# Kernel optimization log

Measured on AMD Instinct MI355X. Metric: run time of the kernel, lower is better.

Reference implementation:

```python
import jax, jax.numpy as jnp
import numpy as np

B_SZ, L_SEQ, H_CH, N_ST = 8, 4096, 256, 64


def setup_inputs() -> dict:
    key = jax.random.key(0)
    ks = jax.random.split(key, 12)
    rn = lambda k, s, sc=1.0: jax.random.normal(k, s, jnp.float32) * sc
    inp = {
        'x': rn(ks[0], (B_SZ, L_SEQ, H_CH)),
        # stable DPLR spectrum: Re(Lambda) < 0, HiPPO-like imaginary ladder
        'Lambda_re': -(jnp.abs(rn(ks[1], (N_ST,))) + 0.1),
        'Lambda_im': jnp.pi * jnp.arange(N_ST, dtype=jnp.float32),
        'P_re': rn(ks[2], (N_ST,), N_ST ** -0.5),
        'P_im': rn(ks[3], (N_ST,), N_ST ** -0.5),
        'Q_re': rn(ks[4], (N_ST,), N_ST ** -0.5),
        'Q_im': rn(ks[5], (N_ST,), N_ST ** -0.5),
        'B_re': rn(ks[6], (N_ST,), N_ST ** -0.5),
        'B_im': rn(ks[7], (N_ST,), N_ST ** -0.5),
        'C_re': rn(ks[8], (H_CH, N_ST), N_ST ** -0.5),
        'C_im': rn(ks[9], (H_CH, N_ST), N_ST ** -0.5),
        'step': jnp.ones((1,), jnp.float32) * 1e-3,
        'D': jnp.zeros((1,), jnp.float32),
        'W_fc': rn(ks[10], (H_CH, H_CH), H_CH ** -0.5),
        'b_fc': jnp.zeros((H_CH,), jnp.float32),
        'ln_g': jnp.ones((H_CH,), jnp.float32),
        'ln_b': jnp.zeros((H_CH,), jnp.float32),
    }
    return inp


def _dplr_kernel(Lambda_re, Lambda_im, P_re, P_im, Q_re, Q_im, B_re, B_im, C_re, C_im, step, L):
    # S4 DPLR generating function evaluated at the L roots of unity (torch_get_K_derta).
    Lam = (Lambda_re + 1j * Lambda_im).astype(jnp.complex64)  # (N,)
    Pc = (P_re + 1j * P_im).astype(jnp.complex64)
    Qc = (Q_re + 1j * Q_im).astype(jnp.complex64)
    Bc = (B_re + 1j * B_im).astype(jnp.complex64)
    Cc = (C_re + 1j * C_im).astype(jnp.complex64)  # (H, N)
    k = jnp.arange(L, dtype=jnp.float32)
    Omega = jnp.exp((-2j * jnp.pi) * (k / L)).astype(jnp.complex64)  # (L,)
    c = 2.0 / (1.0 + Omega)
    g = (2.0 / step[0]) * (1.0 - Omega) / (1.0 + Omega)  # bilinear transform points, (L,)
    inv = 1.0 / (g[:, None] - Lam[None, :])  # Cauchy matrix, (L, N)
    k00 = jnp.einsum('hn,ln->hl', Cc * Bc[None, :], inv)  # (H, L)
    k01 = jnp.einsum('hn,ln->hl', Cc * Pc[None, :], inv)
    k10 = jnp.einsum('n,ln->l', Qc * Bc, inv)  # (L,)
    k11 = jnp.einsum('n,ln->l', Qc * Pc, inv)
    atRoots = c[None, :] * (k00 - k01 * (k10 / (1.0 + k11))[None, :])  # Woodbury correction
    K = jnp.fft.ifft(atRoots, axis=-1).real  # (H, L)
    return K.astype(jnp.float32)


def reference(x, Lambda_re, Lambda_im, P_re, P_im, Q_re, Q_im, B_re, B_im, C_re, C_im, step, D, W_fc, b_fc, ln_g, ln_b):
    Bsz, L, H = x.shape
    step = jnp.maximum(step, 1e-6)
    K = _dplr_kernel(Lambda_re, Lambda_im, P_re, P_im, Q_re, Q_im, B_re, B_im, C_re, C_im, step, L)  # (H, L)
    # causal FFT convolution per channel (torch_convolution with fft=True)
    n = 2 * L
    Kf = jnp.fft.rfft(K, n=n, axis=-1)           # (H, F)
    uf = jnp.fft.rfft(x, n=n, axis=1)            # (B, F, H)
    h1 = jnp.fft.irfft(uf * Kf.T[None], n=n, axis=1)[:, :L, :]
    y1 = jax.nn.gelu(h1 + D * x, approximate=False)  # mult_activation='gelu'
    y2 = jax.nn.gelu(y1 @ W_fc.T + b_fc, approximate=False)  # fc + final_act
    y2 = y2 + x  # skip
    mu = jnp.mean(y2, axis=-1, keepdims=True)
    var = jnp.var(y2, axis=-1, keepdims=True)
    y = (y2 - mu) / jnp.sqrt(var + 1e-5) * ln_g + ln_b  # LayerNorm; dropout p=0
    h_ratio = jnp.max(jnp.abs(y), axis=1) / (jnp.max(jnp.abs(x), axis=1) + 1e-6)  # (B, H)
    return y, h_ratio
```

## Files before the change

### kernel.cpp

```cpp
#include <hip/hip_runtime.h>
#include <math.h>

typedef float2 cf;
typedef float vf2 __attribute__((ext_vector_type(2)));
typedef __attribute__((ext_vector_type(8))) short bf16x8;
typedef __attribute__((ext_vector_type(4))) float f32x4;

__device__ __forceinline__ cf cmk(float x, float y){ cf r; r.x=x; r.y=y; return r; }

__device__ __forceinline__ cf cad(cf a, cf b){
  vf2 av, bv, rv;
  av.x = a.x; av.y = a.y; bv.x = b.x; bv.y = b.y;
  asm("v_pk_add_f32 %0, %1, %2" : "=v"(rv) : "v"(av), "v"(bv));
  return cmk(rv.x, rv.y);
}
__device__ __forceinline__ cf csb(cf a, cf b){
  vf2 av, bv, rv;
  av.x = a.x; av.y = a.y; bv.x = b.x; bv.y = b.y;
  asm("v_pk_add_f32 %0, %1, %2 neg_lo:[0,1] neg_hi:[0,1]" : "=v"(rv) : "v"(av), "v"(bv));
  return cmk(rv.x, rv.y);
}
__device__ __forceinline__ cf cml(cf a, cf b){
  vf2 av, bv, rv;
  av.x = a.x; av.y = a.y; bv.x = b.x; bv.y = b.y;
  asm("v_pk_mul_f32 %0, %1, %2 op_sel:[0,0] op_sel_hi:[0,1]\n\t"
      "v_pk_fma_f32 %0, %1, %2, %0 op_sel:[1,1,0] op_sel_hi:[1,0,1] neg_lo:[1,0,0]"
      : "=&v"(rv) : "v"(av), "v"(bv));
  return cmk(rv.x, rv.y);
}

__device__ __forceinline__ cf cjg(cf a){ return cmk(a.x, -a.y); }
__device__ __forceinline__ cf crcp(cf d){ float r = 1.0f/(d.x*d.x + d.y*d.y); return cmk(d.x*r, -d.y*r); }
__device__ __forceinline__ cf cdv(cf n, cf d){ return cml(n, crcp(d)); }
__device__ __forceinline__ float geluf(float z){ return 0.5f*z*(1.0f + erff(z*0.70710678118654752f)); }

__device__ __forceinline__ cf twid(float f, float sign){
  float h = f * 0.5f;
  float s = __builtin_amdgcn_sinf(h);
  float c0 = __builtin_amdgcn_cosf(h);
  return cmk(c0, sign * s);
}

__device__ __forceinline__ void bfsplit(float v, ushort* h, ushort* l){
  unsigned u = __float_as_uint(v);
  unsigned hr = (u + 0x7FFFu + ((u >> 16) & 1u)) & 0xFFFF0000u;
  *h = (ushort)(hr >> 16);
  float lv = v - __uint_as_float(hr);
  unsigned u2 = __float_as_uint(lv);
  *l = (ushort)((u2 + 0x7FFFu + ((u2 >> 16) & 1u)) >> 16);
}

__device__ __forceinline__ void dif4q(cf& q0, cf& q1, cf& q2, cf& q3, cf w1, float sign){
  cf w2 = cml(w1, w1);
  cf a1 = cad(q0, q2);
  cf c1 = cml(csb(q0, q2), w1);
  cf b1 = cad(q1, q3);
  cf d1 = cml(csb(q1, q3), cmk(-sign*w1.y, sign*w1.x));
  q0 = cad(a1, b1);
  q1 = cml(csb(a1, b1), w2);
  q2 = cad(c1, d1);
  q3 = cml(csb(c1, d1), w2);
}
__device__ __forceinline__ void dit4q(cf& q0, cf& q1, cf& q2, cf& q3, cf w1, float sign){
  cf w2 = cml(w1, w1);
  cf t1 = cml(q1, w2);
  cf a1 = cad(q0, t1), b1 = csb(q0, t1);
  cf t2 = cml(q3, w2);
  cf c1 = cad(q2, t2), d1 = csb(q2, t2);
  cf v1 = cml(c1, w1);
  cf v2 = cml(d1, cmk(-sign*w1.y, sign*w1.x));
  q0 = cad(a1, v1);
  q2 = csb(a1, v1);
  q1 = cad(b1, v2);
  q3 = csb(b1, v2);
}
__device__ __forceinline__ void dif4q0(cf& q0, cf& q1, cf& q2, cf& q3, float sign){
  cf a1 = cad(q0, q2), c1 = csb(q0, q2);
  cf b1 = cad(q1, q3), d0 = csb(q1, q3);
  cf d1 = cmk(-sign*d0.y, sign*d0.x);
  q0 = cad(a1, b1); q1 = csb(a1, b1);
  q2 = cad(c1, d1); q3 = csb(c1, d1);
}
__device__ __forceinline__ void dit4q0(cf& q0, cf& q1, cf& q2, cf& q3, float sign){
  cf a1 = cad(q0, q1), b1 = csb(q0, q1);
  cf c1 = cad(q2, q3), d0 = csb(q2, q3);
  cf v2 = cmk(-sign*d0.y, sign*d0.x);
  q0 = cad(a1, c1); q2 = csb(a1, c1);
  q1 = cad(b1, v2); q3 = csb(b1, v2);
}

__device__ __forceinline__ int brev12(int x){ return (int)(__brev((unsigned)x) >> 20); }
__device__ __forceinline__ int brev13(int x){ return (int)(__brev((unsigned)x) >> 19); }
__device__ __forceinline__ int pidx(int n){ return n + 2*(n>>5); }

template<int N, int SSTART, int TP>
__device__ void fft_dif_r4(cf* __restrict__ a, float sign){
  #pragma unroll
  for (int s = SSTART; s >= 1; s >>= 2){
    __syncthreads();
    #pragma unroll
    for (int g = 0; g < (N >> 2) / TP; g++){
      int w = (int)threadIdx.x + g * TP;
      int j = w & (s - 1);
      int base = ((w & ~(s - 1)) << 2) | j;
      cf A0 = a[base], B0 = a[base + s], C0 = a[base + 2*s], D0 = a[base + 3*s];
      cf w1 = twid((float)j / (float)(2 * s), sign);
      cf w2 = cml(w1, w1);
      cf a1 = cad(A0, C0);
      cf c1 = cml(csb(A0, C0), w1);
      cf b1 = cad(B0, D0);
      cf d1 = cml(csb(B0, D0), cmk(-sign * w1.y, sign * w1.x));
      a[base]         = cad(a1, b1);
      a[base + s]     = cml(csb(a1, b1), w2);
      a[base + 2*s]   = cad(c1, d1);
      a[base + 3*s]   = cml(csb(c1, d1), w2);
    }
  }
  if constexpr ((__builtin_ctz(N) & 1) == 1){
    __syncthreads();
    #pragma unroll
    for (int g = 0; g < (N >> 1) / TP; g++){
      int w = (int)threadIdx.x + g * TP;
      int i = w << 1;
      cf u = a[i], v = a[i + 1];
      a[i] = cad(u, v);
      a[i + 1] = csb(u, v);
    }
  }
  __syncthreads();
}

template<int N, int TP>
__device__ void fft_dit_r4(cf* __restrict__ a, float sign){
  if constexpr ((__builtin_ctz(N) & 1) == 1){
    __syncthreads();
    #pragma unroll
    for (int g = 0; g < (N >> 1) / TP; g++){
      int w = (int)threadIdx.x + g * TP;
      int i = w << 1;
      cf u = a[i], v = a[i + 1];
      a[i] = cad(u, v);
      a[i + 1] = csb(u, v);
    }
  }
  constexpr int S0 = ((__builtin_ctz(N) & 1) == 1) ? 2 : 1;
  #pragma unroll
  for (int s = S0; s <= (N >> 2); s <<= 2){
    __syncthreads();
    #pragma unroll
    for (int g = 0; g < (N >> 2) / TP; g++){
      int w = (int)threadIdx.x + g * TP;
      int j = w & (s - 1);
      int base = ((w & ~(s - 1)) << 2) | j;
      cf A0 = a[base], B0 = a[base + s], C0 = a[base + 2*s], D0 = a[base + 3*s];
      cf w1 = twid((float)j / (float)(2 * s), sign);
      cf w2 = cml(w1, w1);
      cf t1 = cml(B0, w2);
      cf a1 = cad(A0, t1), b1 = csb(A0, t1);
      cf t2 = cml(D0, w2);
      cf c1 = cad(C0, t2), d1 = csb(C0, t2);
      cf v1 = cml(c1, w1);
      cf v2 = cml(d1, cmk(-sign * w1.y, sign * w1.x));
      a[base]         = cad(a1, v1);
      a[base + 2*s]   = csb(a1, v1);
      a[base + s]     = cad(b1, v2);
      a[base + 3*s]   = csb(b1, v2);
    }
  }
  __syncthreads();
}

template<int TP>
__device__ void dif8192_pad_stage(cf* __restrict__ a, float sign){
  __syncthreads();
  #pragma unroll
  for (int g = 0; g < 2048 / TP; g++){
    int w = (int)threadIdx.x + g * TP;
    cf A0 = a[w], B0 = a[w + 2048];
    cf w1 = twid((float)w * (1.0f / 4096.0f), sign);
    cf w2 = cml(w1, w1);
    cf c1 = cml(A0, w1);
    cf d1 = cml(B0, cmk(-sign * w1.y, sign * w1.x));
    a[w]        = cad(A0, B0);
    a[w + 2048] = cml(csb(A0, B0), w2);
    a[w + 4096] = cad(c1, d1);
    a[w + 6144] = cml(csb(c1, d1), w2);
  }
}

__global__ __launch_bounds__(256) void k_transpose_x(const float* __restrict__ x,
                                                     float* __restrict__ xT,
                                                     unsigned* __restrict__ xmax){
  __shared__ float tile[64][65];
  __shared__ float red[64][4];
  int b = blockIdx.z;
  int t0 = blockIdx.x * 64;
  int h0 = blockIdx.y * 64;
  int hc = threadIdx.x & 63, tg = threadIdx.x >> 6;
  float pmax = 0.0f;
  #pragma unroll
  for (int q = 0; q < 16; q++){
    int tr = tg + q * 4;
    float v = x[((size_t)(b * 4096 + t0 + tr)) * 256 + h0 + hc];
    tile[tr][hc] = v;
    pmax = fmaxf(pmax, fabsf(v));
  }
  red[hc][tg] = pmax;
  __syncthreads();
  if (threadIdx.x < 64){
    float m = fmaxf(fmaxf(red[threadIdx.x][0], red[threadIdx.x][1]),
                    fmaxf(red[threadIdx.x][2], red[threadIdx.x][3]));
    atomicMax(&xmax[b * 256 + h0 + threadIdx.x], __float_as_uint(m));
  }
  #pragma unroll
  for (int q = 0; q < 16; q++){
    int hr = tg + q * 4;
    xT[((size_t)(b * 256 + h0 + hr)) * 4096 + t0 + hc] = tile[hc][hr];
  }
}

__global__ void k_wsplit(const float* __restrict__ W, ushort* __restrict__ Wh, ushort* __restrict__ Wl,
                         unsigned* __restrict__ xmax, unsigned* __restrict__ ymax,
                         const float* __restrict__ Cr, const float* __restrict__ Ci,
                         const float* __restrict__ Br, const float* __restrict__ Bi,
                         const float* __restrict__ Pr, const float* __restrict__ Pi,
                         cf* __restrict__ CBt, cf* __restrict__ CPt){
  int i = blockIdx.x * 256 + threadIdx.x;
  if (i < 2048){ xmax[i] = 0u; ymax[i] = 0u; }
  if (i < 16384){
    int n = i >> 8, h = i & 255;
    cf cc = cmk(Cr[h * 64 + n], Ci[h * 64 + n]);
    CBt[i] = cml(cc, cmk(Br[n], Bi[n]));
    CPt[i] = cml(cc, cmk(Pr[n], Pi[n]));
  }
  ushort h, l;
  bfsplit(W[i], &h, &l);
  Wh[i] = h; Wl[i] = l;
}

__global__ __launch_bounds__(256, 2) void k_cauchy(
    const float* __restrict__ Lr, const float* __restrict__ Li,
    const float* __restrict__ Pr, const float* __restrict__ Pi,
    const float* __restrict__ Qr, const float* __restrict__ Qi,
    const float* __restrict__ Br, const float* __restrict__ Bi,
    const cf* __restrict__ CBt, const cf* __restrict__ CPt,
    const float* __restrict__ stepp, cf* __restrict__ A)
{
  __shared__ cf sLam[64], sQB[64], sQP[64];
  __shared__ cf sInv[64][8];
  __shared__ cf sWood[8], sC[8], sG[8];
  int tid = threadIdx.x;
  int l0 = blockIdx.x * 8;
  float stepv = fmaxf(stepp[0], 1e-6f);
  if (tid < 64){
    cf lam = cmk(Lr[tid], Li[tid]);
    cf b = cmk(Br[tid], Bi[tid]);
    cf p = cmk(Pr[tid], Pi[tid]);
    cf q = cmk(Qr[tid], Qi[tid]);
    sLam[tid] = lam;
    sQB[tid] = cml(q, b);
    sQP[tid] = cml(q, p);
  }
  __syncthreads();
  if (tid < 8){
    int l = l0 + tid;
    float ang = -6.2831855f * ((float)l * (1.0f / 4096.0f));
    cf Om = cmk(cosf(ang), sinf(ang));
    cf den = cmk(1.0f + Om.x, Om.y);
    cf num = cmk(1.0f - Om.x, -Om.y);
    cf rden = crcp(den);
    sC[tid] = cml(cmk(2.0f, 0.0f), rden);
    cf g = cml(num, rden);
    float sc = 2.0f / stepv;
    sG[tid] = cmk(g.x * sc, g.y * sc);
  }
  __syncthreads();
  for (int it = tid; it < 512; it += 256){
    int n = it >> 3, ll = it & 7;
    sInv[n][ll] = crcp(csb(sG[ll], sLam[n]));
  }
  __syncthreads();
  if (tid < 8){
    cf k10 = cmk(0,0), k11 = cmk(0,0);
    for (int n = 0; n < 64; n++){
      k10 = cad(k10, cml(sQB[n], sInv[n][tid]));
      k11 = cad(k11, cml(sQP[n], sInv[n][tid]));
    }
    sWood[tid] = cdv(k10, cmk(1.0f + k11.x, k11.y));
  }
  __syncthreads();
  int h = tid;
  cf a0[8], a1[8];
  #pragma unroll
  for (int ll = 0; ll < 8; ll++){ a0[ll] = cmk(0,0); a1[ll] = cmk(0,0); }
  for (int n = 0; n < 64; n++){
    cf cb = CBt[n * 256 + h];
    cf cp = CPt[n * 256 + h];
    #pragma unroll
    for (int ll = 0; ll < 8; ll++){
      cf iv = sInv[n][ll];
      a0[ll] = cad(a0[ll], cml(cb, iv));
      a1[ll] = cad(a1[ll], cml(cp, iv));
    }
  }
  cf* dst = A + (size_t)h * 4096 + l0;
  #pragma unroll
  for (int ll = 0; ll < 8; ll++){
    dst[ll] = cml(sC[ll], csb(a0[ll], cml(a1[ll], sWood[ll])));
  }
}

__global__ __launch_bounds__(1024) void k_kf(const cf* __restrict__ A, float4* __restrict__ Sab){
  extern __shared__ cf c[];
  int hp = blockIdx.x, tid = threadIdx.x;
  const cf* a1p = A + (size_t)(2 * hp) * 4096;
  const cf* a2p = a1p + 4096;
  for (int l = tid; l < 4096; l += 1024){
    int r = brev12(l);
    cf u = a1p[l], w = a2p[l];
    c[r] = cmk(u.x - w.y, u.y + w.x);
  }
  fft_dit_r4<4096, 1024>(c, 1.0f);
  float k1[4], k2[4];
  #pragma unroll
  for (int q = 0; q < 4; q++){
    cf w = c[tid + q * 1024];
    k1[q] = w.x * (1.0f / 4096.0f);
    k2[q] = w.y * (1.0f / 4096.0f);
  }
  __syncthreads();
  #pragma unroll
  for (int q = 0; q < 4; q++) c[tid + q * 1024] = cmk(k1[q], k2[q]);
  dif8192_pad_stage<1024>(c, -1.0f);
  fft_dif_r4<8192, 512, 1024>(c, -1.0f);
  float4* rec = Sab + (size_t)hp * 4097;
  const float sc = 0.5f * 0.5f * (1.0f / 8192.0f);
  #pragma unroll
  for (int q8 = 0; q8 < 4; q8++){
    int t = tid + 1024 * q8;
    int p = t << 1;
    int k = brev13(p);
    int qq = brev13((8192 - k) & 8191);
    cf Zp = c[p], Zq = c[qq];
    float K1x = (Zp.x + Zq.x), K1y = (Zp.y - Zq.y);
    float dx  = (Zp.x - Zq.x), dy  = (Zp.y + Zq.y);
    float K2x = dy, K2y = -dx;
    rec[t] = make_float4((K1x + K2x) * sc, (K1y + K2y) * sc,
                         (K1x - K2x) * sc, (K1y - K2y) * sc);
  }
  if (tid == 0){
    cf Z1 = c[1];
    float K1x = 2.0f * Z1.x, K2x = 2.0f * Z1.y;
    rec[4096] = make_float4((K1x + K2x) * sc, 0.0f, (K1x - K2x) * sc, 0.0f);
  }
}

__global__ __launch_bounds__(256) void k_conv(const float* __restrict__ xT,
                                              const float4* __restrict__ Sab,
                                              const float* __restrict__ Dp,
                                              ushort* __restrict__ y1h,
                                              ushort* __restrict__ y1l){
  __shared__ __align__(16) cf c[8704];
  int blk = blockIdx.x;
  int b = blk >> 7, hp = blk & 127;
  int t = threadIdx.x;
  int lo4 = t & 15, hiT = t >> 4;
  int base0 = lo4 + ((hiT << 1) << 8);
  int base1 = lo4 + ((((hiT << 1) | 1)) << 8);
  int cb0 = pidx((t << 1) << 4);
  int cb1 = pidx(((t << 1) | 1) << 4);
  const float* xs1 = xT + ((size_t)(b * 256 + 2 * hp)) * 4096;
  const float* xs2 = xs1 + 4096;
  cf v[32];
  #pragma unroll
  for (int r = 0; r < 16; r++){
    int n = t + 256 * r;
    v[r] = cmk(xs1[n], xs2[n]);
  }
  #pragma unroll
  for (int r = 0; r < 16; r++)
    v[r + 16] = cml(v[r], twid((float)(t + 256 * r) * (1.0f / 4096.0f), -1.0f));
  #pragma unroll
  for (int r0 = 0; r0 < 4; r0++){
    cf w1 = twid((float)(t + 256 * r0) * (1.0f / 2048.0f), -1.0f);
    dif4q(v[r0], v[r0 + 4], v[r0 + 8], v[r0 + 12], w1, -1.0f);
    dif4q(v[16 + r0], v[16 + r0 + 4], v[16 + r0 + 8], v[16 + r0 + 12], w1, -1.0f);
  }
  {
    cf w1 = twid((float)t * (1.0f / 512.0f), -1.0f);
    #pragma unroll
    for (int g = 0; g < 32; g += 4)
      dif4q(v[g], v[g + 1], v[g + 2], v[g + 3], w1, -1.0f);
  }
  #pragma unroll
  for (int r = 0; r < 32; r++) c[pidx(t + 256 * r)] = v[r];
  __syncthreads();
  #pragma unroll
  for (int u = 0; u < 16; u++){
    v[u]      = c[pidx(base0 + (u << 4))];
    v[16 + u] = c[pidx(base1 + (u << 4))];
  }
  #pragma unroll
  for (int u0 = 0; u0 < 4; u0++){
    cf w1 = twid((float)(lo4 + (u0 << 4)) * (1.0f / 128.0f), -1.0f);
    dif4q(v[u0], v[u0 + 4], v[u0 + 8], v[u0 + 12], w1, -1.0f);
    dif4q(v[16 + u0], v[16 + u0 + 4], v[16 + u0 + 8], v[16 + u0 + 12], w1, -1.0f);
  }
  {
    cf w1 = twid((float)lo4 * (1.0f / 32.0f), -1.0f);
    #pragma unroll
    for (int g = 0; g < 32; g += 4)
      dif4q(v[g], v[g + 1], v[g + 2], v[g + 3], w1, -1.0f);
  }
  #pragma unroll
  for (int u = 0; u < 16; u++){
    c[pidx(base0 + (u << 4))] = v[u];
    c[pidx(base1 + (u << 4))] = v[16 + u];
  }
  __syncthreads();
  #pragma unroll
  for (int k = 0; k < 8; k++){
    float4 q0 = *(const float4*)&c[cb0 + 2 * k];
    float4 q1 = *(const float4*)&c[cb1 + 2 * k];
    v[2 * k]      = cmk(q0.x, q0.y); v[2 * k + 1]      = cmk(q0.z, q0.w);
    v[16 + 2 * k] = cmk(q1.x, q1.y); v[16 + 2 * k + 1] = cmk(q1.z, q1.w);
  }
  #pragma unroll
  for (int u0 = 0; u0 < 4; u0++){
    cf w1 = twid((float)u0 * 0.125f, -1.0f);
    dif4q(v[u0], v[u0 + 4], v[u0 + 8], v[u0 + 12], w1, -1.0f);
    dif4q(v[16 + u0], v[16 + u0 + 4], v[16 + u0 + 8], v[16 + u0 + 12], w1, -1.0f);
  }
  #pragma unroll
  for (int g = 0; g < 32; g += 4) dif4q0(v[g], v[g + 1], v[g + 2], v[g + 3], -1.0f);
  #pragma unroll
  for (int k = 0; k < 8; k++){
    *(float4*)&c[cb0 + 2 * k] = make_float4(v[2*k].x, v[2*k].y, v[2*k+1].x, v[2*k+1].y);
    *(float4*)&c[cb1 + 2 * k] = make_float4(v[16+2*k].x, v[16+2*k].y, v[16+2*k+1].x, v[16+2*k+1].y);
  }
  __syncthreads();
  {
    const float4* rec = Sab + (size_t)hp * 4097;
    #pragma unroll
    for (int q8 = 0; q8 < 16; q8++){
      int th = t + 256 * q8;
      int p = th << 1;
      int k = brev13(p);
      int qq = brev13((8192 - k) & 8191);
      int pi = pidx(p), qi = pidx(qq);
      cf Zp = c[pi], Zq = c[qi];
      float4 r0 = rec[th];
      cf Sap = cmk(r0.x, r0.y), Sbp = cmk(r0.z, r0.w);
      c[pi] = cad(cml(Zp, Sap), cml(cjg(Zq), Sbp));
      c[qi] = cad(cml(Zq, cjg(Sap)), cml(cjg(Zp), cjg(Sbp)));
    }
    if (t == 0){
      float4 e = rec[4096];
      cf Z1 = c[pidx(1)];
      c[pidx(1)] = cad(cml(Z1, cmk(e.x, e.y)), cml(cjg(Z1), cmk(e.z, e.w)));
    }
  }
  __syncthreads();
  #pragma unroll
  for (int k = 0; k < 8; k++){
    float4 q0 = *(const float4*)&c[cb0 + 2 * k];
    float4 q1 = *(const float4*)&c[cb1 + 2 * k];
    v[2 * k]      = cmk(q0.x, q0.y); v[2 * k + 1]      = cmk(q0.z, q0.w);
    v[16 + 2 * k] = cmk(q1.x, q1.y); v[16 + 2 * k + 1] = cmk(q1.z, q1.w);
  }
  #pragma unroll
  for (int g = 0; g < 32; g += 4) dit4q0(v[g], v[g + 1], v[g + 2], v[g + 3], 1.0f);
  #pragma unroll
  for (int u0 = 0; u0 < 4; u0++){
    cf w1 = twid((float)u0 * 0.125f, 1.0f);
    dit4q(v[u0], v[u0 + 4], v[u0 + 8], v[u0 + 12], w1, 1.0f);
    dit4q(v[16 + u0], v[16 + u0 + 4], v[16 + u0 + 8], v[16 + u0 + 12], w1, 1.0f);
  }
  #pragma unroll
  for (int k = 0; k < 8; k++){
    *(float4*)&c[cb0 + 2 * k] = make_float4(v[2*k].x, v[2*k].y, v[2*k+1].x, v[2*k+1].y);
    *(float4*)&c[cb1 + 2 * k] = make_float4(v[16+2*k].x, v[16+2*k].y, v[16+2*k+1].x, v[16+2*k+1].y);
  }
  __syncthreads();
  #pragma unroll
  for (int u = 0; u < 16; u++){
    v[u]      = c[pidx(base0 + (u << 4))];
    v[16 + u] = c[pidx(base1 + (u << 4))];
  }
  {
    cf w1 = twid((float)lo4 * (1.0f / 32.0f), 1.0f);
    #pragma unroll
    for (int g = 0; g < 32; g += 4)
      dit4q(v[g], v[g + 1], v[g + 2], v[g + 3], w1, 1.0f);
  }
  #pragma unroll
  for (int u0 = 0; u0 < 4; u0++){
    cf w1 = twid((float)(lo4 + (u0 << 4)) * (1.0f / 128.0f), 1.0f);
    dit4q(v[u0], v[u0 + 4], v[u0 + 8], v[u0 + 12], w1, 1.0f);
    dit4q(v[16 + u0], v[16 + u0 + 4], v[16 + u0 + 8], v[16 + u0 + 12], w1, 1.0f);
  }
  #pragma unroll
  for (int u = 0; u < 16; u++){
    c[pidx(base0 + (u << 4))] = v[u];
    c[pidx(base1 + (u << 4))] = v[16 + u];
  }
  __syncthreads();
  #pragma unroll
  for (int r = 0; r < 32; r++) v[r] = c[pidx(t + 256 * r)];
  {
    cf w1 = twid((float)t * (1.0f / 512.0f), 1.0f);
    #pragma unroll
    for (int g = 0; g < 32; g += 4)
      dit4q(v[g], v[g + 1], v[g + 2], v[g + 3], w1, 1.0f);
  }
  #pragma unroll
  for (int r0 = 0; r0 < 4; r0++){
    cf w1 = twid((float)(t + 256 * r0) * (1.0f / 2048.0f), 1.0f);
    dit4q(v[r0], v[r0 + 4], v[r0 + 8], v[r0 + 12], w1, 1.0f);
    dit4q(v[16 + r0], v[16 + r0 + 4], v[16 + r0 + 8], v[16 + r0 + 12], w1, 1.0f);
  }
  float Dv = Dp[0];
  size_t base = ((size_t)(b * 256 + 2 * hp)) * 4096;
  #pragma unroll
  for (int r = 0; r < 16; r++){
    int n = t + 256 * r;
    cf w = cad(v[r], cml(v[r + 16], twid((float)n * (1.0f / 4096.0f), 1.0f)));
    float z1 = geluf(fmaf(Dv, xs1[n], w.x));
    float z2 = geluf(fmaf(Dv, xs2[n], w.y));
    ushort h0, l0, h1u, l1;
    bfsplit(z1, &h0, &l0);
    bfsplit(z2, &h1u, &l1);
    y1h[base + n] = h0;         y1l[base + n] = l0;
    y1h[base + 4096 + n] = h1u; y1l[base + 4096 + n] = l1;
  }
}

__global__ __launch_bounds__(256, 3) void k_gemm_ln(
    const ushort* __restrict__ y1h, const ushort* __restrict__ y1l,
    const ushort* __restrict__ Wh, const ushort* __restrict__ Wl,
    const float* __restrict__ bfc, const float* __restrict__ x,
    const float* __restrict__ lng, const float* __restrict__ lnb,
    float* __restrict__ yout, unsigned* __restrict__ ymax)
{
  __shared__ ushort sY[2][64 * 40];
  __shared__ float red1[64][4], red2[64][4];
  int tid = threadIdx.x;
  int l = tid & 63;
  int w = tid >> 6;
  int blk = blockIdx.x;
  int b = blk >> 6;
  int t0 = (blk & 63) * 64;
  int g = l >> 4, cc = l & 15;

  f32x4 acc[4][4];
  #pragma unroll
  for (int m = 0; m < 4; m++)
    #pragma unroll
    for (int n = 0; n < 4; n++)
      acc[m][n] = (f32x4){0.0f, 0.0f, 0.0f, 0.0f};

  int kk = tid >> 3, ts = (tid & 7) * 8;

  #pragma unroll 1
  for (int kc = 0; kc < 256; kc += 32){
    __syncthreads();
    {
      size_t gb = ((size_t)(b * 256 + kc + kk)) * 4096 + t0 + ts;
      float4 vh = *(const float4*)(y1h + gb);
      float4 vl = *(const float4*)(y1l + gb);
      const ushort* ph = (const ushort*)&vh;
      const ushort* pl = (const ushort*)&vl;
      int kblk = kk >> 3, kin = kk & 7;
      #pragma unroll
      for (int e = 0; e < 8; e++){
        int t = ts + e;
        int idx = t * 40 + ((kblk ^ ((t >> 3) & 3)) << 3) + kin;
        sY[0][idx] = ph[e];
        sY[1][idx] = pl[e];
      }
    }
    __syncthreads();
    bf16x8 afh[4], afl[4];
    #pragma unroll
    for (int m = 0; m < 4; m++){
      int t = m * 16 + cc;
      int idx = t * 40 + ((g ^ ((t >> 3) & 3)) << 3);
      afh[m] = *(bf16x8*)&sY[0][idx];
      afl[m] = *(bf16x8*)&sY[1][idx];
    }
    #pragma unroll
    for (int n = 0; n < 4; n++){
      size_t wj = (size_t)(w * 64 + n * 16 + cc) * 256 + kc + g * 8;
      bf16x8 bh = *(const bf16x8*)(Wh + wj);
      bf16x8 bl = *(const bf16x8*)(Wl + wj);
      #pragma unroll
      for (int m = 0; m < 4; m++){
        acc[m][n] = __builtin_amdgcn_mfma_f32_16x16x32_bf16(afh[m], bh, acc[m][n], 0, 0, 0);
        acc[m][n] = __builtin_amdgcn_mfma_f32_16x16x32_bf16(afh[m], bl, acc[m][n], 0, 0, 0);
        acc[m][n] = __builtin_amdgcn_mfma_f32_16x16x32_bf16(afl[m], bh, acc[m][n], 0, 0, 0);
      }
    }
  }

  float bj[4], gj[4], lj[4];
  #pragma unroll
  for (int n = 0; n < 4; n++){
    int j = w * 64 + n * 16 + cc;
    bj[n] = bfc[j]; gj[n] = lng[j]; lj[n] = lnb[j];
  }
  #pragma unroll
  for (int m = 0; m < 4; m++){
    #pragma unroll
    for (int r = 0; r < 4; r++){
      int tl = m * 16 + g * 4 + r;
      size_t rowb = ((size_t)(b * 4096 + t0 + tl)) * 256;
      float ss = 0.0f, sq = 0.0f;
      #pragma unroll
      for (int n = 0; n < 4; n++){
        float z = geluf(acc[m][n][r] + bj[n]) + x[rowb + w * 64 + n * 16 + cc];
        acc[m][n][r] = z;
        ss += z; sq = fmaf(z, z, sq);
      }
      #pragma unroll
      for (int msk = 1; msk < 16; msk <<= 1){
        ss += __shfl_xor(ss, msk);
        sq += __shfl_xor(sq, msk);
      }
      if (cc == 0){ red1[tl][w] = ss; red2[tl][w] = sq; }
    }
  }
  __syncthreads();
  float jm[4] = {0.0f, 0.0f, 0.0f, 0.0f};
  #pragma unroll
  for (int m = 0; m < 4; m++){
    #pragma unroll
    for (int r = 0; r < 4; r++){
      int tl = m * 16 + g * 4 + r;
      float ts1 = red1[tl][0] + red1[tl][1] + red1[tl][2] + red1[tl][3];
      float ts2 = red2[tl][0] + red2[tl][1] + red2[tl][2] + red2[tl][3];
      float mu = ts1 * (1.0f / 256.0f);
      float var = ts2 * (1.0f / 256.0f) - mu * mu;
      float rstd = rsqrtf(var + 1e-5f);
      size_t rowb = ((size_t)(b * 4096 + t0 + tl)) * 256;
      #pragma unroll
      for (int n = 0; n < 4; n++){
        float yv = (acc[m][n][r] - mu) * rstd * gj[n] + lj[n];
        yout[rowb + w * 64 + n * 16 + cc] = yv;
        jm[n] = fmaxf(jm[n], fabsf(yv));
      }
    }
  }
  #pragma unroll
  for (int n = 0; n < 4; n++){
    jm[n] = fmaxf(jm[n], __shfl_xor(jm[n], 16));
    jm[n] = fmaxf(jm[n], __shfl_xor(jm[n], 32));
  }
  if (g == 0){
    #pragma unroll
    for (int n = 0; n < 4; n++)
      atomicMax(&ymax[b * 256 + w * 64 + n * 16 + cc], __float_as_uint(jm[n]));
  }
}

__global__ void k_ratio(const unsigned* __restrict__ ymax, const unsigned* __restrict__ xmax,
                        float* __restrict__ out){
  int i = blockIdx.x * 256 + threadIdx.x;
  if (i < 2048){
    float ym = __uint_as_float(ymax[i]);
    float xm = __uint_as_float(xmax[i]);
    out[8388608 + i] = ym / (xm + 1e-6f);
  }
}

extern "C" void kernel_launch(void* const* d_in, const int* in_sizes, int n_in,
                              void* d_out, int out_size, void* d_ws, size_t ws_size,
                              hipStream_t stream)
{
  const float* x    = (const float*)d_in[0];
  const float* Lr   = (const float*)d_in[1];
  const float* Li   = (const float*)d_in[2];
  const float* Pr   = (const float*)d_in[3];
  const float* Pi   = (const float*)d_in[4];
  const float* Qr   = (const float*)d_in[5];
  const float* Qi   = (const float*)d_in[6];
  const float* Br   = (const float*)d_in[7];
  const float* Bi   = (const float*)d_in[8];
  const float* Cr   = (const float*)d_in[9];
  const float* Ci   = (const float*)d_in[10];
  const float* stp  = (const float*)d_in[11];
  const float* Dp   = (const float*)d_in[12];
  const float* Wfc  = (const float*)d_in[13];
  const float* bfc  = (const float*)d_in[14];
  const float* lng  = (const float*)d_in[15];
  const float* lnb  = (const float*)d_in[16];

  char* ws = (char*)d_ws;
  float*    xT   = (float*)(ws);
  float4*   Sab  = (float4*)(ws + ((size_t)32 << 20));
  cf*       A    = (cf*)(ws + ((size_t)41 << 20));
  ushort*   y1h  = (ushort*)(ws + ((size_t)41 << 20));
  ushort*   y1l  = (ushort*)(ws + ((size_t)57 << 20));
  ushort*   Wh   = (ushort*)(ws + ((size_t)73 << 20));
  ushort*   Wl   = (ushort*)(ws + ((size_t)73 << 20) + (128u << 10));
  unsigned* xmax = (unsigned*)(ws + ((size_t)73 << 20) + (256u << 10));
  unsigned* ymax = xmax + 2048;
  cf*       CBt  = (cf*)(ws + ((size_t)74 << 20));
  cf*       CPt  = (cf*)(ws + ((size_t)74 << 20) + (128u << 10));

  k_wsplit<<<256, 256, 0, stream>>>(Wfc, Wh, Wl, xmax, ymax, Cr, Ci, Br, Bi, Pr, Pi, CBt, CPt);
  dim3 gt(64, 4, 8);
  k_transpose_x<<<gt, 256, 0, stream>>>(x, xT, xmax);
  k_cauchy<<<512, 256, 0, stream>>>(Lr, Li, Pr, Pi, Qr, Qi, Br, Bi, CBt, CPt, stp, A);
  k_kf<<<128, 1024, 65536, stream>>>(A, Sab);
  k_conv<<<1024, 256, 0, stream>>>(xT, Sab, Dp, y1h, y1l);
  k_gemm_ln<<<512, 256, 0, stream>>>(y1h, y1l, Wh, Wl, bfc, x, lng, lnb, (float*)d_out, ymax);
  k_ratio<<<8, 256, 0, stream>>>(ymax, xmax, (float*)d_out);
}
```

Baseline: 173.2 us.

## Restructure FFT convolution kernel to 512 threads with shuffle-based radix-2 stage

```diff
diff --git a/kernel.cpp b/kernel.cpp
--- a/kernel.cpp
+++ b/kernel.cpp
@@ -39,6 +39,10 @@
   float s = __builtin_amdgcn_sinf(h);
   float c0 = __builtin_amdgcn_cosf(h);
   return cmk(c0, sign * s);
+}
+
+__device__ __forceinline__ cf shflx(cf v, int m){
+  return cmk(__shfl_xor(v.x, m), __shfl_xor(v.y, m));
 }
 
 __device__ __forceinline__ void bfsplit(float v, ushort* h, ushort* l){
@@ -91,7 +95,7 @@
 
 __device__ __forceinline__ int brev12(int x){ return (int)(__brev((unsigned)x) >> 20); }
 __device__ __forceinline__ int brev13(int x){ return (int)(__brev((unsigned)x) >> 19); }
-__device__ __forceinline__ int pidx(int n){ return n + 2*(n>>5); }
+__device__ __forceinline__ int pidx(int n){ return n + 6*(n>>5); }
 
 template<int N, int SSTART, int TP>
 __device__ void fft_dif_r4(cf* __restrict__ a, float sign){
@@ -355,95 +359,94 @@
   }
 }
 
-__global__ __launch_bounds__(256) void k_conv(const float* __restrict__ xT,
+__global__ __launch_bounds__(512) void k_conv(const float* __restrict__ xT,
                                               const float4* __restrict__ Sab,
                                               const float* __restrict__ Dp,
                                               ushort* __restrict__ y1h,
                                               ushort* __restrict__ y1l){
-  __shared__ __align__(16) cf c[8704];
+  __shared__ __align__(16) cf c[9728];
   int blk = blockIdx.x;
   int b = blk >> 7, hp = blk & 127;
   int t = threadIdx.x;
-  int lo4 = t & 15, hiT = t >> 4;
-  int base0 = lo4 + ((hiT << 1) << 8);
-  int base1 = lo4 + ((((hiT << 1) | 1)) << 8);
-  int cb0 = pidx((t << 1) << 4);
-  int cb1 = pidx(((t << 1) | 1) << 4);
+  int cl = t & 31;
+  int m1b = (t >> 5) * 512 + cl;
+  int cb  = pidx(t << 4);
   const float* xs1 = xT + ((size_t)(b * 256 + 2 * hp)) * 4096;
   const float* xs2 = xs1 + 4096;
-  cf v[32];
-  #pragma unroll
-  for (int r = 0; r < 16; r++){
-    int n = t + 256 * r;
+  cf v[16];
+  #pragma unroll
+  for (int r = 0; r < 8; r++){
+    int n = t + 512 * r;
     v[r] = cmk(xs1[n], xs2[n]);
   }
   #pragma unroll
-  for (int r = 0; r < 16; r++)
-    v[r + 16] = cml(v[r], twid((float)(t + 256 * r) * (1.0f / 4096.0f), -1.0f));
-  #pragma unroll
-  for (int r0 = 0; r0 < 4; r0++){
-    cf w1 = twid((float)(t + 256 * r0) * (1.0f / 2048.0f), -1.0f);
-    dif4q(v[r0], v[r0 + 4], v[r0 + 8], v[r0 + 12], w1, -1.0f);
-    dif4q(v[16 + r0], v[16 + r0 + 4], v[16 + r0 + 8], v[16 + r0 + 12], w1, -1.0f);
+  for (int r = 0; r < 8; r++)
+    v[r + 8] = cml(v[r], twid((float)(t + 512 * r) * (1.0f / 4096.0f), -1.0f));
+  #pragma unroll
+  for (int r0 = 0; r0 < 2; r0++){
+    cf w1 = twid((float)(t + 512 * r0) * (1.0f / 2048.0f), -1.0f);
+    dif4q(v[r0], v[r0 + 2], v[r0 + 4], v[r0 + 6], w1, -1.0f);
+    dif4q(v[8 + r0], v[8 + r0 + 2], v[8 + r0 + 4], v[8 + r0 + 6], w1, -1.0f);
   }
   {
-    cf w1 = twid((float)t * (1.0f / 512.0f), -1.0f);
-    #pragma unroll
-    for (int g = 0; g < 32; g += 4)
+    cf tw = twid((float)t * (1.0f / 512.0f), -1.0f);
+    #pragma unroll
+    for (int g = 0; g < 16; g += 2){
+      cf lo = cad(v[g], v[g + 1]);
+      cf hi = cml(csb(v[g], v[g + 1]), tw);
+      v[g] = lo; v[g + 1] = hi;
+    }
+  }
+  #pragma unroll
+  for (int r = 0; r < 16; r++) c[pidx(t + 512 * r)] = v[r];
+  __syncthreads();
+  #pragma unroll
+  for (int u = 0; u < 16; u++) v[u] = c[pidx(m1b + u * 32)];
+  #pragma unroll
+  for (int u0 = 0; u0 < 4; u0++){
+    cf w1 = twid((float)(cl + 32 * u0) * (1.0f / 256.0f), -1.0f);
+    dif4q(v[u0], v[u0 + 4], v[u0 + 8], v[u0 + 12], w1, -1.0f);
+  }
+  {
+    cf w1 = twid((float)cl * (1.0f / 64.0f), -1.0f);
+    #pragma unroll
+    for (int g = 0; g < 16; g += 4)
       dif4q(v[g], v[g + 1], v[g + 2], v[g + 3], w1, -1.0f);
   }
   #pragma unroll
-  for (int r = 0; r < 32; r++) c[pidx(t + 256 * r)] = v[r];
-  __syncthreads();
-  #pragma unroll
-  for (int u = 0; u < 16; u++){
-    v[u]      = c[pidx(base0 + (u << 4))];
-    v[16 + u] = c[pidx(base1 + (u << 4))];
-  }
-  #pragma unroll
-  for (int u0 = 0; u0 < 4; u0++){
-    cf w1 = twid((float)(lo4 + (u0 << 4)) * (1.0f / 128.0f), -1.0f);
-    dif4q(v[u0], v[u0 + 4], v[u0 + 8], v[u0 + 12], w1, -1.0f);
-    dif4q(v[16 + u0], v[16 + u0 + 4], v[16 + u0 + 8], v[16 + u0 + 12], w1, -1.0f);
+  for (int u = 0; u < 16; u++) c[pidx(m1b + u * 32)] = v[u];
+  __syncthreads();
+  #pragma unroll
+  for (int k = 0; k < 8; k++){
+    float4 q0 = *(const float4*)&c[cb + 2 * k];
+    v[2 * k]     = cmk(q0.x, q0.y);
+    v[2 * k + 1] = cmk(q0.z, q0.w);
   }
   {
-    cf w1 = twid((float)lo4 * (1.0f / 32.0f), -1.0f);
-    #pragma unroll
-    for (int g = 0; g < 32; g += 4)
-      dif4q(v[g], v[g + 1], v[g + 2], v[g + 3], w1, -1.0f);
-  }
-  #pragma unroll
-  for (int u = 0; u < 16; u++){
-    c[pidx(base0 + (u << 4))] = v[u];
-    c[pidx(base1 + (u << 4))] = v[16 + u];
-  }
-  __syncthreads();
-  #pragma unroll
-  for (int k = 0; k < 8; k++){
-    float4 q0 = *(const float4*)&c[cb0 + 2 * k];
-    float4 q1 = *(const float4*)&c[cb1 + 2 * k];
-    v[2 * k]      = cmk(q0.x, q0.y); v[2 * k + 1]      = cmk(q0.z, q0.w);
-    v[16 + 2 * k] = cmk(q1.x, q1.y); v[16 + 2 * k + 1] = cmk(q1.z, q1.w);
+    bool hb = (t & 1) != 0;
+    #pragma unroll
+    for (int u2 = 0; u2 < 16; u2++){
+      cf o = shflx(v[u2], 1);
+      cf tw = twid((float)u2 * (1.0f / 16.0f), -1.0f);
+      v[u2] = hb ? cml(csb(o, v[u2]), tw) : cad(v[u2], o);
+    }
   }
   #pragma unroll
   for (int u0 = 0; u0 < 4; u0++){
     cf w1 = twid((float)u0 * 0.125f, -1.0f);
     dif4q(v[u0], v[u0 + 4], v[u0 + 8], v[u0 + 12], w1, -1.0f);
-    dif4q(v[16 + u0], v[16 + u0 + 4], v[16 + u0 + 8], v[16 + u0 + 12], w1, -1.0f);
-  }
-  #pragma unroll
-  for (int g = 0; g < 32; g += 4) dif4q0(v[g], v[g + 1], v[g + 2], v[g + 3], -1.0f);
-  #pragma unroll
-  for (int k = 0; k < 8; k++){
-    *(float4*)&c[cb0 + 2 * k] = make_float4(v[2*k].x, v[2*k].y, v[2*k+1].x, v[2*k+1].y);
-    *(float4*)&c[cb1 + 2 * k] = make_float4(v[16+2*k].x, v[16+2*k].y, v[16+2*k+1].x, v[16+2*k+1].y);
-  }
+  }
+  #pragma unroll
+  for (int g = 0; g < 16; g += 4) dif4q0(v[g], v[g + 1], v[g + 2], v[g + 3], -1.0f);
+  #pragma unroll
+  for (int k = 0; k < 8; k++)
+    *(float4*)&c[cb + 2 * k] = make_float4(v[2*k].x, v[2*k].y, v[2*k+1].x, v[2*k+1].y);
   __syncthreads();
   {
     const float4* rec = Sab + (size_t)hp * 4097;
     #pragma unroll
-    for (int q8 = 0; q8 < 16; q8++){
-      int th = t + 256 * q8;
+    for (int q8 = 0; q8 < 8; q8++){
+      int th = t + 512 * q8;
       int p = th << 1;
       int k = brev13(p);
       int qq = brev13((8192 - k) & 8191);
@@ -463,68 +466,71 @@
   __syncthreads();
   #pragma unroll
   for (int k = 0; k < 8; k++){
-    float4 q0 = *(const float4*)&c[cb0 + 2 * k];
-    float4 q1 = *(const float4*)&c[cb1 + 2 * k];
-    v[2 * k]      = cmk(q0.x, q0.y); v[2 * k + 1]      = cmk(q0.z, q0.w);
-    v[16 + 2 * k] = cmk(q1.x, q1.y); v[16 + 2 * k + 1] = cmk(q1.z, q1.w);
-  }
-  #pragma unroll
-  for (int g = 0; g < 32; g += 4) dit4q0(v[g], v[g + 1], v[g + 2], v[g + 3], 1.0f);
+    float4 q0 = *(const float4*)&c[cb + 2 * k];
+    v[2 * k]     = cmk(q0.x, q0.y);
+    v[2 * k + 1] = cmk(q0.z, q0.w);
+  }
+  #pragma unroll
+  for (int g = 0; g < 16; g += 4) dit4q0(v[g], v[g + 1], v[g + 2], v[g + 3], 1.0f);
   #pragma unroll
   for (int u0 = 0; u0 < 4; u0++){
     cf w1 = twid((float)u0 * 0.125f, 1.0f);
     dit4q(v[u0], v[u0 + 4], v[u0 + 8], v[u0 + 12], w1, 1.0f);
-    dit4q(v[16 + u0], v[16 + u0 + 4], v[16 + u0 + 8], v[16 + u0 + 12], w1, 1.0f);
-  }
-  #pragma unroll
-  for (int k = 0; k < 8; k++){
-    *(float4*)&c[cb0 + 2 * k] = make_float4(v[2*k].x, v[2*k].y, v[2*k+1].x, v[2*k+1].y);
-    *(float4*)&c[cb1 + 2 * k] = make_float4(v[16+2*k].x, v[16+2*k].y, v[16+2*k+1].x, v[16+2*k+1].y);
-  }
-  __syncthreads();
-  #pragma unroll
-  for (int u = 0; u < 16; u++){
-    v[u]      = c[pidx(base0 + (u << 4))];
-    v[16 + u] = c[pidx(base1 + (u << 4))];
   }
   {
-    cf w1 = twid((float)lo4 * (1.0f / 32.0f), 1.0f);
-    #pragma unroll
-    for (int g = 0; g < 32; g += 4)
+    bool hb = (t & 1) != 0;
+    #pragma unroll
+    for (int u2 = 0; u2 < 16; u2++){
+      cf o = shflx(v[u2], 1);
+      cf w = twid((float)u2 * (1.0f / 16.0f), 1.0f);
+      cf whv = cml(w, hb ? v[u2] : o);
+      v[u2] = hb ? csb(o, whv) : cad(v[u2], whv);
+    }
+  }
+  #pragma unroll
+  for (int k = 0; k < 8; k++)
+    *(float4*)&c[cb + 2 * k] = make_float4(v[2*k].x, v[2*k].y, v[2*k+1].x, v[2*k+1].y);
+  __syncthreads();
+  #pragma unroll
+  for (int u = 0; u < 16; u++) v[u] = c[pidx(m1b + u * 32)];
+  {
+    cf w1 = twid((float)cl * (1.0f / 64.0f), 1.0f);
+    #pragma unroll
+    for (int g = 0; g < 16; g += 4)
       dit4q(v[g], v[g + 1], v[g + 2], v[g + 3], w1, 1.0f);
   }
   #pragma unroll
   for (int u0 = 0; u0 < 4; u0++){
-    cf w1 = twid((float)(lo4 + (u0 << 4)) * (1.0f / 128.0f), 1.0f);
+    cf w1 = twid((float)(cl + 32 * u0) * (1.0f / 256.0f), 1.0f);
     dit4q(v[u0], v[u0 + 4], v[u0 + 8], v[u0 + 12], w1, 1.0f);
-    dit4q(v[16 + u0], v[16 + u0 + 4], v[16 + u0 + 8], v[16 + u0 + 12], w1, 1.0f);
-  }
-  #pragma unroll
-  for (int u = 0; u < 16; u++){
-    c[pidx(base0 + (u << 4))] = v[u];
-    c[pidx(base1 + (u << 4))] = v[16 + u];
-  }
-  __syncthreads();
-  #pragma unroll
-  for (int r = 0; r < 32; r++) v[r] = c[pidx(t + 256 * r)];
+  }
+  #pragma unroll
+  for (int u = 0; u < 16; u++) c[pidx(m1b + u * 32)] = v[u];
+  __syncthreads();
+  #pragma unroll
+  for (int r = 0; r < 16; r++) v[r] = c[pidx(t + 512 * r)];
   {
-    cf w1 = twid((float)t * (1.0f / 512.0f), 1.0f);
-    #pragma unroll
-    for (int g = 0; g < 32; g += 4)
-      dit4q(v[g], v[g + 1], v[g + 2], v[g + 3], w1, 1.0f);
-  }
-  #pragma unroll
-  for (int r0 = 0; r0 < 4; r0++){
-    cf w1 = twid((float)(t + 256 * r0) * (1.0f / 2048.0f), 1.0f);
-    dit4q(v[r0], v[r0 + 4], v[r0 + 8], v[r0 + 12], w1, 1.0f);
-    dit4q(v[16 + r0], v[16 + r0 + 4], v[16 + r0 + 8], v[16 + r0 + 12], w1, 1.0f);
+    cf tw = twid((float)t * (1.0f / 512.0f), 1.0f);
+    #pragma unroll
+    for (int g = 0; g < 16; g += 2){
+      cf tb = cml(v[g + 1], tw);
+      cf a0 = v[g];
+      v[g] = cad(a0, tb);
+      v[g + 1] = csb(a0, tb);
+    }
+  }
+  #pragma unroll
+  for (int r0 = 0; r0 < 2; r0++){
+    cf w1 = twid((float)(t + 512 * r0) * (1.0f / 2048.0f), 1.0f);
+    dit4q(v[r0], v[r0 + 2], v[r0 + 4], v[r0 + 6], w1, 1.0f);
+    dit4q(v[8 + r0], v[8 + r0 + 2], v[8 + r0 + 4], v[8 + r0 + 6], w1, 1.0f);
   }
   float Dv = Dp[0];
   size_t base = ((size_t)(b * 256 + 2 * hp)) * 4096;
   #pragma unroll
-  for (int r = 0; r < 16; r++){
-    int n = t + 256 * r;
-    cf w = cad(v[r], cml(v[r + 16], twid((float)n * (1.0f / 4096.0f), 1.0f)));
+  for (int r = 0; r < 8; r++){
+    int n = t + 512 * r;
+    cf w = cad(v[r], cml(v[r + 8], twid((float)n * (1.0f / 4096.0f), 1.0f)));
     float z1 = geluf(fmaf(Dv, xs1[n], w.x));
     float z2 = geluf(fmaf(Dv, xs2[n], w.y));
     ushort h0, l0, h1u, l1;
@@ -712,7 +718,7 @@
   k_transpose_x<<<gt, 256, 0, stream>>>(x, xT, xmax);
   k_cauchy<<<512, 256, 0, stream>>>(Lr, Li, Pr, Pi, Qr, Qi, Br, Bi, CBt, CPt, stp, A);
   k_kf<<<128, 1024, 65536, stream>>>(A, Sab);
-  k_conv<<<1024, 256, 0, stream>>>(xT, Sab, Dp, y1h, y1l);
+  k_conv<<<1024, 512, 0, stream>>>(xT, Sab, Dp, y1h, y1l);
   k_gemm_ln<<<512, 256, 0, stream>>>(y1h, y1l, Wh, Wl, bfc, x, lng, lnb, (float*)d_out, ymax);
   k_ratio<<<8, 256, 0, stream>>>(ymax, xmax, (float*)d_out);
 }
```

New measurement: 175.2 us. No clear change (+1.2%).
